# Optimization experiments

Hardware: AMD Instinct MI355X
Metric: run time of the kernel (lower is better)

The kernel has to match this reference:

```python
import jax, jax.numpy as jnp
import numpy as np

H = 8          # heads
D = 512        # d_model
DK = D // H    # per-head dim
FF = 2048      # feed-forward size
STACKS = 3
VOCAB = 5000
PAD = 0
LN_EPS = 1e-6


def _layer_norm(x, g, b):
    mu = jnp.mean(x, axis=-1, keepdims=True)
    var = jnp.mean(jnp.square(x - mu), axis=-1, keepdims=True)
    return (x - mu) * jax.lax.rsqrt(var + LN_EPS) * g + b


def _positional_encoding(T, d):
    pos = jnp.arange(T, dtype=jnp.float32)[:, None]                      # (T,1)
    div = jnp.exp(jnp.arange(0, d, 2, dtype=jnp.float32) * (-np.log(10000.0) / d))
    pe = jnp.zeros((T, d), dtype=jnp.float32)
    pe = pe.at[:, 0::2].set(jnp.sin(pos * div))
    pe = pe.at[:, 1::2].set(jnp.cos(pos * div))
    return pe  # (T, D)


def _mha(q_in, kv, wq, bq, wk, bk, wv, bv, wo, bo, mask):
    B, Tq, _ = q_in.shape
    Tk = kv.shape[1]
    q = (q_in @ wq + bq).reshape(B, Tq, H, DK).transpose(0, 2, 1, 3)   # (B,H,Tq,DK)
    k = (kv @ wk + bk).reshape(B, Tk, H, DK).transpose(0, 2, 1, 3)
    v = (kv @ wv + bv).reshape(B, Tk, H, DK).transpose(0, 2, 1, 3)
    score = jnp.einsum('bhqd,bhkd->bhqk', q, k) / jnp.sqrt(jnp.float32(DK))
    if mask is not None:
        score = jnp.where(mask, score, jnp.float32(-1e9))
    p = jax.nn.softmax(score, axis=-1)
    out = jnp.einsum('bhqk,bhkd->bhqd', p, v)
    out = out.transpose(0, 2, 1, 3).reshape(B, Tq, D)
    return out @ wo + bo


def setup_inputs() -> dict:
    key = jax.random.key(0)
    ks = jax.random.split(key, 24)
    s = 0.02
    inp = {
        'target': jax.random.randint(ks[0], (32, 256), 0, VOCAB),
        'memory': jax.random.normal(ks[1], (32, 1024, D), dtype=jnp.float32),
        'emb': jax.random.normal(ks[2], (VOCAB, D), dtype=jnp.float32) * s,
        'ln_g': jnp.ones((D,), jnp.float32),
        'ln_b': jnp.zeros((D,), jnp.float32),
        'ff_w1': jax.random.normal(ks[3], (D, FF), jnp.float32) * s,
        'ff_b1': jnp.zeros((FF,), jnp.float32),
        'ff_w2': jax.random.normal(ks[4], (FF, D), jnp.float32) * s,
        'ff_b2': jnp.zeros((D,), jnp.float32),
    }
    names = ['wq', 'wk', 'wv', 'wo']
    for i, n in enumerate(names):
        inp['sa_' + n] = jax.random.normal(ks[5 + i], (D, D), jnp.float32) * s
        inp['sa_b' + n[1]] = jnp.zeros((D,), jnp.float32)
        inp['ca_' + n] = jax.random.normal(ks[9 + i], (D, D), jnp.float32) * s
        inp['ca_b' + n[1]] = jnp.zeros((D,), jnp.float32)
    return inp


def reference(target, memory, emb, ln_g, ln_b, ff_w1, ff_b1, ff_w2, ff_b2,
              sa_wq, sa_bq, sa_wk, sa_bk, sa_wv, sa_bv, sa_wo, sa_bo,
              ca_wq, ca_bq, ca_wk, ca_bk, ca_wv, ca_bv, ca_wo, ca_bo):
    B, T = target.shape
    x = emb[target] * jnp.sqrt(jnp.float32(D))              # (B,T,D)
    x = x + _positional_encoding(T, D)                       # dropout = identity (eval)
    # masks: causal & pad for self-attn; cross-attn mask is all-ones -> skip
    pad = (target != PAD)[:, None, :, None]                  # (B,1,T,1)
    causal = jnp.tril(jnp.ones((T, T), dtype=bool))          # (T,T)
    tgt_mask = pad & causal                                  # (B,1,T,T)
    out = x
    for _ in range(STACKS):  # shared parameters
        n = _layer_norm(out, ln_g, ln_b)
        out = out + _mha(n, n, sa_wq, sa_bq, sa_wk, sa_bk, sa_wv, sa_bv, sa_wo, sa_bo, tgt_mask)
        n = _layer_norm(out, ln_g, ln_b)
        out = out + _mha(n, memory, ca_wq, ca_bq, ca_wk, ca_bk, ca_wv, ca_bv, ca_wo, ca_bo, None)
        n = _layer_norm(out, ln_g, ln_b)
        out = out + (jax.nn.relu(n @ ff_w1 + ff_b1) @ ff_w2 + ff_b2)
    return _layer_norm(out, ln_g, ln_b)
```

## Files before the change

kernel.cpp:

```cpp
#include <hip/hip_runtime.h>
#include <cstdint>
#include <cstddef>

typedef unsigned short u16;
typedef __bf16 bf16x8 __attribute__((ext_vector_type(8)));
typedef float f32x4 __attribute__((ext_vector_type(4)));

#define DEV static __device__ __forceinline__

#define QSCALE 0.18033688011112042f

DEV u16 f2bf(float f) { unsigned v; __builtin_memcpy(&v, &f, 4); v += 0x7fffu + ((v >> 16) & 1u); return (u16)(v >> 16); }

DEV void gll16(const void* g, void* l) {
    __builtin_amdgcn_global_load_lds(
        (__attribute__((address_space(1))) void*)g,
        (__attribute__((address_space(3))) void*)l, 16, 0, 0);
}

__global__ void embed_pe(const int* __restrict__ tgt, const float* __restrict__ emb,
                         float* __restrict__ x)
{
    const int bt = blockIdx.x;
    const int t  = bt & 255;
    const int tok = tgt[bt];
    for (int d = threadIdx.x; d < 512; d += 256) {
        float e  = emb[(size_t)tok * 512 + d] * 22.62741699796952f;
        int   d0 = d & ~1;
        float ang = (float)t * expf((float)d0 * (-9.210340371976184f / 512.f));
        float pe  = (d & 1) ? cosf(ang) : sinf(ang);
        x[(size_t)bt * 512 + d] = e + pe;
    }
}

__global__ void transpose_k(const float* __restrict__ in, u16* __restrict__ out,
                            int K, int N)
{
    int id = blockIdx.x * 256 + threadIdx.x;
    int k = id / N, n = id % N;
    out[(size_t)n * K + k] = f2bf(in[id]);
}

__global__ void memcast(const float* __restrict__ in, u16* __restrict__ out)
{
    int i = (blockIdx.x * 256 + threadIdx.x) * 4;
    float4 v = *(const float4*)(in + i);
    uint2 w;
    w.x = (unsigned)f2bf(v.x) | ((unsigned)f2bf(v.y) << 16);
    w.y = (unsigned)f2bf(v.z) | ((unsigned)f2bf(v.w) << 16);
    *(uint2*)(out + i) = w;
}

__global__ void concat_bias(const float* __restrict__ a, const float* __restrict__ b,
                            float* __restrict__ out)
{
    int i = blockIdx.x * 256 + threadIdx.x;
    if (i < 512) { out[i] = a[i]; out[512 + i] = b[i]; }
}

template<bool OUTF32>
__global__ void layernorm_k(const float* __restrict__ x, const float* __restrict__ g,
                            const float* __restrict__ b, void* __restrict__ outv)
{
    const int row  = blockIdx.x * 4 + (threadIdx.x >> 6);
    const int lane = threadIdx.x & 63;
    const float* xr = x + (size_t)row * 512;
    float4 v0 = *(const float4*)(xr + lane * 4);
    float4 v1 = *(const float4*)(xr + 256 + lane * 4);
    float s = v0.x + v0.y + v0.z + v0.w + v1.x + v1.y + v1.z + v1.w;
    float q = v0.x*v0.x + v0.y*v0.y + v0.z*v0.z + v0.w*v0.w
            + v1.x*v1.x + v1.y*v1.y + v1.z*v1.z + v1.w*v1.w;
#pragma unroll
    for (int o = 1; o < 64; o <<= 1) { s += __shfl_xor(s, o, 64); q += __shfl_xor(q, o, 64); }
    float mu  = s * (1.f / 512.f);
    float var = q * (1.f / 512.f) - mu * mu;
    float rs  = rsqrtf(fmaxf(var, 0.f) + 1e-6f);

#pragma unroll
    for (int h = 0; h < 2; h++) {
        const int d0 = h * 256 + lane * 4;
        float4 v = h ? v1 : v0;
        float4 gg = *(const float4*)(g + d0);
        float4 bb = *(const float4*)(b + d0);
        float o0 = (v.x - mu) * rs * gg.x + bb.x;
        float o1 = (v.y - mu) * rs * gg.y + bb.y;
        float o2 = (v.z - mu) * rs * gg.z + bb.z;
        float o3 = (v.w - mu) * rs * gg.w + bb.w;
        if (OUTF32) {
            *(float4*)((float*)outv + (size_t)row * 512 + d0) = make_float4(o0, o1, o2, o3);
        } else {
            uint2 w;
            w.x = (unsigned)f2bf(o0) | ((unsigned)f2bf(o1) << 16);
            w.y = (unsigned)f2bf(o2) | ((unsigned)f2bf(o3) << 16);
            *(uint2*)((u16*)outv + (size_t)row * 512 + d0) = w;
        }
    }
}

template<int EPI, bool BROW, int BN, int QS, int SPLIT>
__launch_bounds__(256, BN == 64 ? 4 : 2)
__global__ void gemm_bt(const u16* __restrict__ A, int lda,
                        const u16* __restrict__ Bt,
                        const float* __restrict__ bias,
                        void* __restrict__ outp, int ldo, int K)
{
    constexpr int NJ = BN / 32;
    __shared__ u16 As[128 * 32];
    __shared__ u16 Bs[BN * 32];

    const int gx = gridDim.x, gy = gridDim.y;
    const int nwg = gx * gy * gridDim.z;
    int lin = blockIdx.x + gx * (blockIdx.y + gy * blockIdx.z);
    lin = (lin & 7) * (nwg >> 3) + (lin >> 3);
    const int bx = lin % gx;
    const int rem = lin / gx;
    const int by = rem % gy;
    const int bz = rem / gy;

    const int tid  = threadIdx.x;
    const int lane = tid & 63;
    const int wave = tid >> 6;
    const int quad = lane >> 4, l16 = lane & 15;
    const int l4 = lane >> 2, c8 = (lane & 3) * 8;
    const int m0 = by * 128, n0 = bx * BN;
    const int wm = (wave >> 1) * 64, wn = (wave & 1) * (BN / 2);

    const int kc = K / SPLIT;
    const int kbeg = bz * kc;

    f32x4 acc[4][NJ];
#pragma unroll
    for (int i = 0; i < 4; i++)
#pragma unroll
        for (int j = 0; j < NJ; j++) acc[i][j] = f32x4{0.f, 0.f, 0.f, 0.f};

    for (int k0 = kbeg; k0 < kbeg + kc; k0 += 32) {
        __syncthreads();
        gll16(&A[(size_t)(m0 + wave * 32 + l4)      * lda + k0 + c8], &As[(wave * 32) * 32]);
        gll16(&A[(size_t)(m0 + wave * 32 + 16 + l4) * lda + k0 + c8], &As[(wave * 32 + 16) * 32]);
        if (BN == 128) {
            gll16(&Bt[(size_t)(n0 + wave * 32 + l4)      * K + k0 + c8], &Bs[(wave * 32) * 32]);
            gll16(&Bt[(size_t)(n0 + wave * 32 + 16 + l4) * K + k0 + c8], &Bs[(wave * 32 + 16) * 32]);
        } else {
            gll16(&Bt[(size_t)(n0 + wave * 16 + l4) * K + k0 + c8], &Bs[(wave * 16) * 32]);
        }
        __syncthreads();
        bf16x8 af[4], bfr[NJ];
#pragma unroll
        for (int i = 0; i < 4; i++) af[i]  = *(const bf16x8*)&As[(wm + i * 16 + l16) * 32 + quad * 8];
#pragma unroll
        for (int j = 0; j < NJ; j++) bfr[j] = *(const bf16x8*)&Bs[(wn + j * 16 + l16) * 32 + quad * 8];
#pragma unroll
        for (int i = 0; i < 4; i++)
#pragma unroll
            for (int j = 0; j < NJ; j++)
                acc[i][j] = __builtin_amdgcn_mfma_f32_16x16x32_bf16(af[i], bfr[j], acc[i][j], 0, 0, 0);
    }

    const bool dobias = (SPLIT == 1) || (bz == 0);
#pragma unroll
    for (int i = 0; i < 4; i++)
#pragma unroll
        for (int j = 0; j < NJ; j++) {
            const int col = n0 + wn + j * 16 + l16;
            const float bc = BROW ? 0.f : (dobias ? bias[col] : 0.f);
#pragma unroll
            for (int r = 0; r < 4; r++) {
                const int row = m0 + wm + i * 16 + quad * 4 + r;
                const float bv = BROW ? (dobias ? bias[row] : 0.f) : bc;
                float v = acc[i][j][r] + bv;
                if (QS == 1) v *= QSCALE;
                if (QS == 2 && col < 512) v *= QSCALE;
                if (EPI == 1) v = fmaxf(v, 0.f);
                if (EPI == 2) {
                    if (SPLIT > 1) atomicAdd((float*)outp + (size_t)row * ldo + col, v);
                    else           ((float*)outp)[(size_t)row * ldo + col] += v;
                } else {
                    ((u16*)outp)[(size_t)row * ldo + col] = f2bf(v);
                }
            }
        }
}

template<bool SELF>
__launch_bounds__(256, 4)
__global__ void attn(const u16* __restrict__ Qb, int qs,
                     const u16* __restrict__ Kb, int ks, int koff,
                     const u16* __restrict__ Vt, int ldv,
                     const int* __restrict__ target,
                     u16* __restrict__ Ob, int Tk)
{
    __shared__ u16 KsL[64 * 32], KsH[64 * 32];
    __shared__ u16 VsL[64 * 32], VsH[64 * 32];
    __shared__ float P32[4][16][68];
    __shared__ int needtail;
    const int tid  = threadIdx.x;
    const int lane = tid & 63;
    const int wave = tid >> 6;
    const int quad = lane >> 4, l16 = lane & 15;
    const int l4 = lane >> 2, c8 = (lane & 3) * 8;
    const int b = blockIdx.x, h = blockIdx.y, qz = blockIdx.z;
    const int qbase = qz * 64 + wave * 16;
    const int hq = h * 64;

    if (tid == 0) needtail = 0;

    const u16* qr = Qb + (size_t)(b * 256 + qbase + l16) * qs + hq;
    bf16x8 qf0 = *(const bf16x8*)(qr + quad * 8);
    bf16x8 qf1 = *(const bf16x8*)(qr + 32 + quad * 8);

    f32x4 o[4];
#pragma unroll
    for (int t = 0; t < 4; t++) o[t] = f32x4{0.f, 0.f, 0.f, 0.f};
    float ps = 0.f;
    bool rv[4];
    bool inv = false;
    if (SELF) {
#pragma unroll
        for (int r = 0; r < 4; r++) {
            rv[r] = (target[b * 256 + qbase + quad * 4 + r] != 0);
            inv |= !rv[r];
        }
    }
    const bool winv = SELF ? __any(inv) : false;
    __syncthreads();
    if (winv && lane == 0) needtail = 1;
    __syncthreads();
    const int nch = SELF ? (needtail ? (Tk >> 6) : (qz + 1)) : (Tk >> 6);

    const u16* kbase = Kb + (size_t)b * Tk * ks + koff + hq;
    const u16* vbase = Vt + (size_t)hq * ldv + (size_t)b * Tk;
    float* pw = &P32[wave][0][0];

    for (int c = 0; c < nch; c++) {
        const int k0 = c * 64;
        __syncthreads();
        gll16(kbase + (size_t)(k0 + wave * 16 + l4) * ks + c8,      &KsL[(wave * 16) * 32]);
        gll16(kbase + (size_t)(k0 + wave * 16 + l4) * ks + 32 + c8, &KsH[(wave * 16) * 32]);
        gll16(vbase + (size_t)(wave * 16 + l4) * ldv + k0 + c8,      &VsL[(wave * 16) * 32]);
        gll16(vbase + (size_t)(wave * 16 + l4) * ldv + k0 + 32 + c8, &VsH[(wave * 16) * 32]);
        __syncthreads();

        float s[4][4];
#pragma unroll
        for (int g = 0; g < 4; g++) {
            bf16x8 kf0 = *(const bf16x8*)&KsL[(g * 16 + l16) * 32 + quad * 8];
            bf16x8 kf1 = *(const bf16x8*)&KsH[(g * 16 + l16) * 32 + quad * 8];
            f32x4 sv = f32x4{0.f, 0.f, 0.f, 0.f};
            sv = __builtin_amdgcn_mfma_f32_16x16x32_bf16(qf0, kf0, sv, 0, 0, 0);
            sv = __builtin_amdgcn_mfma_f32_16x16x32_bf16(qf1, kf1, sv, 0, 0, 0);
#pragma unroll
            for (int r = 0; r < 4; r++) s[g][r] = sv[r];
        }
        if (SELF) {
            if (k0 + 64 > qbase) {
#pragma unroll
                for (int g = 0; g < 4; g++)
#pragma unroll
                    for (int r = 0; r < 4; r++)
                        if (k0 + g * 16 + l16 > qbase + quad * 4 + r) s[g][r] = -1e9f;
            }
            if (winv) {
#pragma unroll
                for (int g = 0; g < 4; g++)
#pragma unroll
                    for (int r = 0; r < 4; r++)
                        if (!rv[r]) s[g][r] = 0.f;
            }
        }
#pragma unroll
        for (int g = 0; g < 4; g++)
#pragma unroll
            for (int r = 0; r < 4; r++)
                pw[(quad * 4 + r) * 68 + g * 16 + l16] = s[g][r];
        f32x4 ra0 = *(const f32x4*)&pw[l16 * 68 + quad * 8];
        f32x4 ra1 = *(const f32x4*)&pw[l16 * 68 + quad * 8 + 4];
        f32x4 rb0 = *(const f32x4*)&pw[l16 * 68 + 32 + quad * 8];
        f32x4 rb1 = *(const f32x4*)&pw[l16 * 68 + 36 + quad * 8];
        bf16x8 pa0, pa1;
#pragma unroll
        for (int j = 0; j < 4; j++) { float p = exp2f(ra0[j]); ps += p; pa0[j]     = (__bf16)p; }
#pragma unroll
        for (int j = 0; j < 4; j++) { float p = exp2f(ra1[j]); ps += p; pa0[4 + j] = (__bf16)p; }
#pragma unroll
        for (int j = 0; j < 4; j++) { float p = exp2f(rb0[j]); ps += p; pa1[j]     = (__bf16)p; }
#pragma unroll
        for (int j = 0; j < 4; j++) { float p = exp2f(rb1[j]); ps += p; pa1[4 + j] = (__bf16)p; }
#pragma unroll
        for (int t = 0; t < 4; t++) {
            bf16x8 vf0 = *(const bf16x8*)&VsL[(t * 16 + l16) * 32 + quad * 8];
            bf16x8 vf1 = *(const bf16x8*)&VsH[(t * 16 + l16) * 32 + quad * 8];
            o[t] = __builtin_amdgcn_mfma_f32_16x16x32_bf16(pa0, vf0, o[t], 0, 0, 0);
            o[t] = __builtin_amdgcn_mfma_f32_16x16x32_bf16(pa1, vf1, o[t], 0, 0, 0);
        }
    }

    ps += __shfl_xor(ps, 16, 64);
    ps += __shfl_xor(ps, 32, 64);
#pragma unroll
    for (int r = 0; r < 4; r++) {
        const float inv_l = 1.f / __shfl(ps, quad * 4 + r, 64);
        const int tq = qbase + quad * 4 + r;
        u16* orow = Ob + (size_t)(b * 256 + tq) * 512 + hq;
#pragma unroll
        for (int t = 0; t < 4; t++) orow[t * 16 + l16] = f2bf(o[t][r] * inv_l);
    }
}

#define O_X      ((size_t)0)
#define O_N      ((size_t)16777216)
#define O_QK     ((size_t)25165824)
#define O_VTS    ((size_t)41943040)
#define O_ATT    ((size_t)50331648)
#define O_FFN    ((size_t)58720256)
#define O_KVC    ((size_t)92274688)
#define O_VTC    ((size_t)125829120)
#define O_WQKT   ((size_t)159383552)
#define O_SAVT   ((size_t)160432128)
#define O_WOT    ((size_t)160956416)
#define O_CAQT   ((size_t)161480704)
#define O_CAKT   ((size_t)162004992)
#define O_CAVT   ((size_t)162529280)
#define O_CAWOT  ((size_t)163053568)
#define O_FF1T   ((size_t)163577856)
#define O_FF2T   ((size_t)165675008)
#define O_BQK    ((size_t)167772160)

extern "C" void kernel_launch(void* const* d_in, const int* in_sizes, int n_in,
                              void* d_out, int out_size, void* d_ws, size_t ws_size,
                              hipStream_t stream)
{
    const int*   target = (const int*)d_in[0];
    const float* memory = (const float*)d_in[1];
    const float* emb    = (const float*)d_in[2];
    const float* ln_g   = (const float*)d_in[3];
    const float* ln_b   = (const float*)d_in[4];
    const float* ff_w1  = (const float*)d_in[5];
    const float* ff_b1  = (const float*)d_in[6];
    const float* ff_w2  = (const float*)d_in[7];
    const float* ff_b2  = (const float*)d_in[8];
    const float* sa_wq  = (const float*)d_in[9];
    const float* sa_bq  = (const float*)d_in[10];
    const float* ca_wq  = (const float*)d_in[11];
    const float* ca_bq  = (const float*)d_in[12];
    const float* sa_wk  = (const float*)d_in[13];
    const float* sa_bk  = (const float*)d_in[14];
    const float* ca_wk  = (const float*)d_in[15];
    const float* ca_bk  = (const float*)d_in[16];
    const float* sa_wv  = (const float*)d_in[17];
    const float* sa_bv  = (const float*)d_in[18];
    const float* ca_wv  = (const float*)d_in[19];
    const float* ca_bv  = (const float*)d_in[20];
    const float* sa_wo  = (const float*)d_in[21];
    const float* sa_bo  = (const float*)d_in[22];
    const float* ca_wo  = (const float*)d_in[23];
    const float* ca_bo  = (const float*)d_in[24];

    char* ws = (char*)d_ws;
    float* xf   = (float*)(ws + O_X);
    u16* nbuf   = (u16*)(ws + O_N);
    u16* qk     = (u16*)(ws + O_QK);
    u16* qbuf   = (u16*)(ws + O_QK);
    u16* vts    = (u16*)(ws + O_VTS);
    u16* att    = (u16*)(ws + O_ATT);
    u16* ffn    = (u16*)(ws + O_FFN);
    u16* membf  = (u16*)(ws + O_FFN);
    u16* kvc    = (u16*)(ws + O_KVC);
    u16* vtc    = (u16*)(ws + O_VTC);
    u16* wqkt   = (u16*)(ws + O_WQKT);
    u16* savt   = (u16*)(ws + O_SAVT);
    u16* wot    = (u16*)(ws + O_WOT);
    u16* caqt   = (u16*)(ws + O_CAQT);
    u16* cakt   = (u16*)(ws + O_CAKT);
    u16* cavt   = (u16*)(ws + O_CAVT);
    u16* cawot  = (u16*)(ws + O_CAWOT);
    u16* ff1t   = (u16*)(ws + O_FF1T);
    u16* ff2t   = (u16*)(ws + O_FF2T);
    float* bqk  = (float*)(ws + O_BQK);

    transpose_k<<<1024, 256, 0, stream>>>(sa_wq, wqkt,             512, 512);
    transpose_k<<<1024, 256, 0, stream>>>(sa_wk, wqkt + 512 * 512, 512, 512);
    transpose_k<<<1024, 256, 0, stream>>>(sa_wv, savt,  512, 512);
    transpose_k<<<1024, 256, 0, stream>>>(sa_wo, wot,   512, 512);
    transpose_k<<<1024, 256, 0, stream>>>(ca_wq, caqt,  512, 512);
    transpose_k<<<1024, 256, 0, stream>>>(ca_wk, cakt,  512, 512);
    transpose_k<<<1024, 256, 0, stream>>>(ca_wv, cavt,  512, 512);
    transpose_k<<<1024, 256, 0, stream>>>(ca_wo, cawot, 512, 512);
    transpose_k<<<4096, 256, 0, stream>>>(ff_w1, ff1t,  512, 2048);
    transpose_k<<<4096, 256, 0, stream>>>(ff_w2, ff2t, 2048, 512);
    concat_bias<<<2, 256, 0, stream>>>(sa_bq, sa_bk, bqk);

    embed_pe<<<8192, 256, 0, stream>>>(target, emb, xf);

    memcast<<<16384, 256, 0, stream>>>(memory, membf);
    gemm_bt<0, false, 128, 0, 1><<<dim3(4, 256), 256, 0, stream>>>(membf, 512, cakt, ca_bk, kvc, 512, 512);
    gemm_bt<0, true,  128, 0, 1><<<dim3(256, 4), 256, 0, stream>>>(cavt, 512, membf, ca_bv, vtc, 32768, 512);

    for (int s = 0; s < 3; s++) {
        layernorm_k<false><<<2048, 256, 0, stream>>>(xf, ln_g, ln_b, nbuf);
        gemm_bt<0, false, 64, 2, 1><<<dim3(16, 64), 256, 0, stream>>>(nbuf, 512, wqkt, bqk, qk, 1024, 512);
        gemm_bt<0, true,  64, 0, 1><<<dim3(128, 4), 256, 0, stream>>>(savt, 512, nbuf, sa_bv, vts, 8192, 512);
        attn<true><<<dim3(32, 8, 4), 256, 0, stream>>>(qk, 1024, qk, 1024, 512, vts, 8192, target, att, 256);
        gemm_bt<2, false, 64, 0, 2><<<dim3(8, 64, 2), 256, 0, stream>>>(att, 512, wot, sa_bo, xf, 512, 512);
        layernorm_k<false><<<2048, 256, 0, stream>>>(xf, ln_g, ln_b, nbuf);
        gemm_bt<0, false, 64, 1, 1><<<dim3(8, 64), 256, 0, stream>>>(nbuf, 512, caqt, ca_bq, qbuf, 512, 512);
        attn<false><<<dim3(32, 8, 4), 256, 0, stream>>>(qbuf, 512, kvc, 512, 0, vtc, 32768, nullptr, att, 1024);
        gemm_bt<2, false, 64, 0, 2><<<dim3(8, 64, 2), 256, 0, stream>>>(att, 512, cawot, ca_bo, xf, 512, 512);
        layernorm_k<false><<<2048, 256, 0, stream>>>(xf, ln_g, ln_b, nbuf);
        gemm_bt<1, false, 64, 0, 1><<<dim3(32, 64), 256, 0, stream>>>(nbuf, 512, ff1t, ff_b1, ffn, 2048, 512);
        gemm_bt<2, false, 64, 0, 4><<<dim3(8, 64, 4), 256, 0, stream>>>(ffn, 2048, ff2t, ff_b2, xf, 512, 2048);
    }

    layernorm_k<true><<<2048, 256, 0, stream>>>(xf, ln_g, ln_b, d_out);
}
```

Measured before the change: 1.091 ms.

## Replace atomic split-K residual adds with partial buffers summed in fused layernorm

Split-K output-projection and FFN2 GEMMs now write their two partial results to separate fp32 buffers instead of atomically adding into the residual stream. A new layernorm kernel sums the residual with both partials, writes the updated residual, and normalizes in one pass. FFN2 split-K drops from 4 to 2. The cross-attention K/V precompute GEMMs also switch from 128-wide to 64-wide tiles. This removes the atomic traffic and the read-modify-write of the residual, at the cost of extra partial-buffer writes and reads and workspace aliasing that must not conflict.

```diff
diff --git a/kernel.cpp b/kernel.cpp
--- a/kernel.cpp
+++ b/kernel.cpp
@@ -97,6 +97,59 @@
     }
 }
 
+template<bool OUTF32>
+__global__ void ln_sum_k(const float* __restrict__ x, const float* __restrict__ p,
+                         const float* __restrict__ g, const float* __restrict__ b,
+                         float* __restrict__ xout, void* __restrict__ outv)
+{
+    const int row  = blockIdx.x * 4 + (threadIdx.x >> 6);
+    const int lane = threadIdx.x & 63;
+    const size_t base = (size_t)row * 512;
+    const float* xr = x + base;
+    const float* pa = p + base;
+    const float* pb = p + 4194304 + base;
+    float4 v0, v1;
+    {
+        float4 a = *(const float4*)(xr + lane * 4);
+        float4 c = *(const float4*)(pa + lane * 4);
+        float4 d = *(const float4*)(pb + lane * 4);
+        v0 = make_float4(a.x + c.x + d.x, a.y + c.y + d.y, a.z + c.z + d.z, a.w + c.w + d.w);
+        a = *(const float4*)(xr + 256 + lane * 4);
+        c = *(const float4*)(pa + 256 + lane * 4);
+        d = *(const float4*)(pb + 256 + lane * 4);
+        v1 = make_float4(a.x + c.x + d.x, a.y + c.y + d.y, a.z + c.z + d.z, a.w + c.w + d.w);
+    }
+    float s = v0.x + v0.y + v0.z + v0.w + v1.x + v1.y + v1.z + v1.w;
+    float q = v0.x*v0.x + v0.y*v0.y + v0.z*v0.z + v0.w*v0.w
+            + v1.x*v1.x + v1.y*v1.y + v1.z*v1.z + v1.w*v1.w;
+#pragma unroll
+    for (int o = 1; o < 64; o <<= 1) { s += __shfl_xor(s, o, 64); q += __shfl_xor(q, o, 64); }
+    float mu  = s * (1.f / 512.f);
+    float var = q * (1.f / 512.f) - mu * mu;
+    float rs  = rsqrtf(fmaxf(var, 0.f) + 1e-6f);
+
+#pragma unroll
+    for (int h = 0; h < 2; h++) {
+        const int d0 = h * 256 + lane * 4;
+        float4 v = h ? v1 : v0;
+        if (!OUTF32) *(float4*)(xout + base + d0) = v;
+        float4 gg = *(const float4*)(g + d0);
+        float4 bb = *(const float4*)(b + d0);
+        float o0 = (v.x - mu) * rs * gg.x + bb.x;
+        float o1 = (v.y - mu) * rs * gg.y + bb.y;
+        float o2 = (v.z - mu) * rs * gg.z + bb.z;
+        float o3 = (v.w - mu) * rs * gg.w + bb.w;
+        if (OUTF32) {
+            *(float4*)((float*)outv + base + d0) = make_float4(o0, o1, o2, o3);
+        } else {
+            uint2 w;
+            w.x = (unsigned)f2bf(o0) | ((unsigned)f2bf(o1) << 16);
+            w.y = (unsigned)f2bf(o2) | ((unsigned)f2bf(o3) << 16);
+            *(uint2*)((u16*)outv + base + d0) = w;
+        }
+    }
+}
+
 template<int EPI, bool BROW, int BN, int QS, int SPLIT>
 __launch_bounds__(256, BN == 64 ? 4 : 2)
 __global__ void gemm_bt(const u16* __restrict__ A, int lda,
@@ -172,9 +225,8 @@
                 if (QS == 1) v *= QSCALE;
                 if (QS == 2 && col < 512) v *= QSCALE;
                 if (EPI == 1) v = fmaxf(v, 0.f);
-                if (EPI == 2) {
-                    if (SPLIT > 1) atomicAdd((float*)outp + (size_t)row * ldo + col, v);
-                    else           ((float*)outp)[(size_t)row * ldo + col] += v;
+                if (EPI == 3) {
+                    ((float*)outp)[(size_t)bz * 8192 * ldo + (size_t)row * ldo + col] = v;
                 } else {
                     ((u16*)outp)[(size_t)row * ldo + col] = f2bf(v);
                 }
@@ -361,10 +413,12 @@
     u16* nbuf   = (u16*)(ws + O_N);
     u16* qk     = (u16*)(ws + O_QK);
     u16* qbuf   = (u16*)(ws + O_QK);
+    float* ffp  = (float*)(ws + O_QK);
     u16* vts    = (u16*)(ws + O_VTS);
     u16* att    = (u16*)(ws + O_ATT);
     u16* ffn    = (u16*)(ws + O_FFN);
     u16* membf  = (u16*)(ws + O_FFN);
+    float* wop  = (float*)(ws + O_FFN);
     u16* kvc    = (u16*)(ws + O_KVC);
     u16* vtc    = (u16*)(ws + O_VTC);
     u16* wqkt   = (u16*)(ws + O_WQKT);
@@ -393,23 +447,26 @@
     embed_pe<<<8192, 256, 0, stream>>>(target, emb, xf);
 
     memcast<<<16384, 256, 0, stream>>>(memory, membf);
-    gemm_bt<0, false, 128, 0, 1><<<dim3(4, 256), 256, 0, stream>>>(membf, 512, cakt, ca_bk, kvc, 512, 512);
-    gemm_bt<0, true,  128, 0, 1><<<dim3(256, 4), 256, 0, stream>>>(cavt, 512, membf, ca_bv, vtc, 32768, 512);
+    gemm_bt<0, false, 64, 0, 1><<<dim3(8, 256), 256, 0, stream>>>(membf, 512, cakt, ca_bk, kvc, 512, 512);
+    gemm_bt<0, true,  64, 0, 1><<<dim3(512, 4), 256, 0, stream>>>(cavt, 512, membf, ca_bv, vtc, 32768, 512);
 
     for (int s = 0; s < 3; s++) {
-        layernorm_k<false><<<2048, 256, 0, stream>>>(xf, ln_g, ln_b, nbuf);
+        if (s == 0)
+            layernorm_k<false><<<2048, 256, 0, stream>>>(xf, ln_g, ln_b, nbuf);
+        else
+            ln_sum_k<false><<<2048, 256, 0, stream>>>(xf, ffp, ln_g, ln_b, xf, nbuf);
         gemm_bt<0, false, 64, 2, 1><<<dim3(16, 64), 256, 0, stream>>>(nbuf, 512, wqkt, bqk, qk, 1024, 512);
         gemm_bt<0, true,  64, 0, 1><<<dim3(128, 4), 256, 0, stream>>>(savt, 512, nbuf, sa_bv, vts, 8192, 512);
         attn<true><<<dim3(32, 8, 4), 256, 0, stream>>>(qk, 1024, qk, 1024, 512, vts, 8192, target, att, 256);
-        gemm_bt<2, false, 64, 0, 2><<<dim3(8, 64, 2), 256, 0, stream>>>(att, 512, wot, sa_bo, xf, 512, 512);
-        layernorm_k<false><<<2048, 256, 0, stream>>>(xf, ln_g, ln_b, nbuf);
+        gemm_bt<3, false, 64, 0, 2><<<dim3(8, 64, 2), 256, 0, stream>>>(att, 512, wot, sa_bo, wop, 512, 512);
+        ln_sum_k<false><<<2048, 256, 0, stream>>>(xf, wop, ln_g, ln_b, xf, nbuf);
         gemm_bt<0, false, 64, 1, 1><<<dim3(8, 64), 256, 0, stream>>>(nbuf, 512, caqt, ca_bq, qbuf, 512, 512);
         attn<false><<<dim3(32, 8, 4), 256, 0, stream>>>(qbuf, 512, kvc, 512, 0, vtc, 32768, nullptr, att, 1024);
-        gemm_bt<2, false, 64, 0, 2><<<dim3(8, 64, 2), 256, 0, stream>>>(att, 512, cawot, ca_bo, xf, 512, 512);
-        layernorm_k<false><<<2048, 256, 0, stream>>>(xf, ln_g, ln_b, nbuf);
+        gemm_bt<3, false, 64, 0, 2><<<dim3(8, 64, 2), 256, 0, stream>>>(att, 512, cawot, ca_bo, wop, 512, 512);
+        ln_sum_k<false><<<2048, 256, 0, stream>>>(xf, wop, ln_g, ln_b, xf, nbuf);
         gemm_bt<1, false, 64, 0, 1><<<dim3(32, 64), 256, 0, stream>>>(nbuf, 512, ff1t, ff_b1, ffn, 2048, 512);
-        gemm_bt<2, false, 64, 0, 4><<<dim3(8, 64, 4), 256, 0, stream>>>(ffn, 2048, ff2t, ff_b2, xf, 512, 2048);
-    }
-
-    layernorm_k<true><<<2048, 256, 0, stream>>>(xf, ln_g, ln_b, d_out);
-}
+        gemm_bt<3, false, 64, 0, 2><<<dim3(8, 64, 2), 256, 0, stream>>>(ffn, 2048, ff2t, ff_b2, ffp, 512, 2048);
+    }
+
+    ln_sum_k<true><<<2048, 256, 0, stream>>>(xf, ffp, ln_g, ln_b, xf, d_out);
+}
```

New measurement: 926.1 us. 15.1% less time.
